# Performance work log

Measured on AMD Instinct MI355X. Metric: run time of the kernel, lower is better.

## Reference

```python
import jax, jax.numpy as jnp
import numpy as np

N_NODES = 50000
K_NEIGH = 32
D_IN = 128
D_OUT = 128
LEAKY_ALPHA = 0.2  # tf.nn.leaky_relu default


def setup_inputs() -> dict:
    key = jax.random.key(0)
    k1, k2, k3, k4 = jax.random.split(key, 4)
    glorot = lambda k, shape: jax.random.uniform(
        k, shape, jnp.float32, -1.0, 1.0) * np.sqrt(6.0 / (shape[0] + shape[1]))
    return {
        "self_vecs": jax.random.normal(k1, (N_NODES, D_IN), jnp.float32),
        "neigh_vecs": jax.random.normal(k2, (N_NODES * K_NEIGH, D_IN), jnp.float32),
        "feat_weights": glorot(k3, (D_IN, D_OUT)),
        "attn_weights": glorot(k4, (D_OUT, 1)),
        "bias": jnp.zeros((D_OUT,), jnp.float32),
        "num_neighbors": K_NEIGH,
    }


def reference(self_vecs, neigh_vecs, feat_weights, attn_weights, bias, num_neighbors):
    n = self_vecs.shape[0]
    from_neighs = neigh_vecs @ feat_weights            # [N*K, Dout]
    h_self = self_vecs @ feat_weights                  # [N, Dout]
    neigh_logits = (from_neighs @ attn_weights).reshape(n, num_neighbors)  # [N, K]
    self_logits = h_self @ attn_weights                # [N, 1]
    logits = neigh_logits + self_logits                # [N, K]
    coefs = jax.nn.softmax(jax.nn.leaky_relu(logits, LEAKY_ALPHA), axis=-1)
    # dropout rate = 0.0 -> identity
    h_neighs = jnp.einsum("nk,nkd->nd", coefs,
                          from_neighs.reshape(n, num_neighbors, -1))  # [N, Dout]
    return jax.nn.relu(h_self + h_neighs + bias)
```

## Files before the change

kernel.cpp:

```cpp
#include <hip/hip_runtime.h>


constexpr int D   = 128;
constexpr int KN  = 32;
constexpr int LDX = 136;

typedef __bf16 bf16;
typedef __attribute__((ext_vector_type(8))) __bf16 bf16x8;
typedef __attribute__((ext_vector_type(4))) float  f32x4;

__global__ void prep_kernel(const float* __restrict__ W,
                            const float* __restrict__ attn,
                            bf16* __restrict__ Wt,
                            float* __restrict__ wa)
{
  const int i = blockIdx.x * 256 + threadIdx.x;
  if (i < D * D) {
    const int n = i >> 7, k = i & 127;
    Wt[i] = (bf16)W[(k << 7) + n];
  }
  if (i < D) {
    float s = 0.f;
    for (int n = 0; n < D; ++n) s += W[i * D + n] * attn[n];
    wa[i] = s;
  }
}

__global__ __launch_bounds__(64, 3)
void gat_pass1(const float* __restrict__ selfv,
               const float* __restrict__ neighv,
               const float* __restrict__ Wfp,
               const float* __restrict__ attnv,
               const float* __restrict__ wa_g,
               float* __restrict__ ybuf,
               int nnodes, int npn, int use_ws)
{
  __shared__ __align__(16) bf16 Xs[KN * LDX];
  __shared__ __align__(16) bf16 wab[D];

  const int lane = threadIdx.x;
  const int q = lane >> 4, l15 = lane & 15;

  float wa0, wa1;
  if (use_ws) {
    float2 w2 = *(const float2*)&wa_g[2 * lane];
    wa0 = w2.x; wa1 = w2.y;
  } else {
    float s0 = 0.f, s1 = 0.f;
    for (int n = 0; n < D; ++n) {
      const float an = attnv[n];
      s0 += Wfp[(2 * lane) * D + n] * an;
      s1 += Wfp[(2 * lane + 1) * D + n] * an;
    }
    wa0 = s0; wa1 = s1;
  }
  wab[2 * lane]     = (bf16)wa0;
  wab[2 * lane + 1] = (bf16)wa1;

  const float4* neigh4 = (const float4*)neighv;
  const float2* self2  = (const float2*)selfv;
  const int base = blockIdx.x * npn;
  if (base >= nnodes) return;

  float4 st[16];
  float2 selfr;
  {
    const float4* p = neigh4 + (size_t)base * (KN * D / 4);
    #pragma unroll
    for (int c = 0; c < 8; ++c) {
      st[2 * c]     = p[2 * (lane + 64 * c)];
      st[2 * c + 1] = p[2 * (lane + 64 * c) + 1];
    }
    selfr = self2[(size_t)base * (D / 2) + lane];
  }

  for (int i = 0; i < npn; ++i) {
    const int node = base + i;
    if (node >= nnodes) break;

    #pragma unroll
    for (int c = 0; c < 8; ++c) {
      const int cc = lane + 64 * c;
      const int row = cc >> 4, c8 = cc & 15;
      const float4 va = st[2 * c], vb = st[2 * c + 1];
      bf16x8 b = { (bf16)va.x, (bf16)va.y, (bf16)va.z, (bf16)va.w,
                   (bf16)vb.x, (bf16)vb.y, (bf16)vb.z, (bf16)vb.w };
      *(bf16x8*)&Xs[row * LDX + c8 * 8] = b;
    }
    const float2 sv = selfr;

    if (i + 1 < npn && node + 1 < nnodes) {
      const float4* p = neigh4 + (size_t)(node + 1) * (KN * D / 4);
      #pragma unroll
      for (int c = 0; c < 8; ++c) {
        st[2 * c]     = p[2 * (lane + 64 * c)];
        st[2 * c + 1] = p[2 * (lane + 64 * c) + 1];
      }
      selfr = self2[(size_t)(node + 1) * (D / 2) + lane];
    }

    f32x4 acc0 = {0.f, 0.f, 0.f, 0.f}, acc1 = {0.f, 0.f, 0.f, 0.f};
    #pragma unroll
    for (int ks = 0; ks < 4; ++ks) {
      const bf16x8 B  = *(const bf16x8*)&wab[ks * 32 + q * 8];
      const bf16x8 A0 = *(const bf16x8*)&Xs[l15 * LDX + ks * 32 + q * 8];
      const bf16x8 A1 = *(const bf16x8*)&Xs[(16 + l15) * LDX + ks * 32 + q * 8];
      acc0 = __builtin_amdgcn_mfma_f32_16x16x32_bf16(A0, B, acc0, 0, 0, 0);
      acc1 = __builtin_amdgcn_mfma_f32_16x16x32_bf16(A1, B, acc1, 0, 0, 0);
    }

    float sl = sv.x * wa0 + sv.y * wa1;
    sl += __shfl_xor(sl, 1);  sl += __shfl_xor(sl, 2);  sl += __shfl_xor(sl, 4);
    sl += __shfl_xor(sl, 8);  sl += __shfl_xor(sl, 16); sl += __shfl_xor(sl, 32);

    float e0[4], e1[4], mx = -3.4e38f;
    #pragma unroll
    for (int r = 0; r < 4; ++r) {
      float t0 = acc0[r] + sl; t0 = t0 > 0.f ? t0 : 0.2f * t0;
      float t1 = acc1[r] + sl; t1 = t1 > 0.f ? t1 : 0.2f * t1;
      e0[r] = t0; e1[r] = t1;
      mx = fmaxf(mx, fmaxf(t0, t1));
    }
    mx = fmaxf(mx, __shfl_xor(mx, 16));
    mx = fmaxf(mx, __shfl_xor(mx, 32));
    float s = 0.f;
    #pragma unroll
    for (int r = 0; r < 4; ++r) {
      e0[r] = __expf(e0[r] - mx); e1[r] = __expf(e1[r] - mx);
      s += e0[r] + e1[r];
    }
    s += __shfl_xor(s, 16); s += __shfl_xor(s, 32);
    const float inv = 1.0f / s;
    #pragma unroll
    for (int r = 0; r < 4; ++r) { e0[r] *= inv; e1[r] *= inv; }

    float cf[32];
    #pragma unroll
    for (int k = 0; k < 32; ++k) {
      const int src = ((k >> 2) & 3) * 16;
      const float v = (k < 16) ? e0[k & 3] : e1[k & 3];
      cf[k] = __int_as_float(__builtin_amdgcn_readlane(__float_as_int(v), src));
    }

    float z0 = 0.f, z1 = 0.f;
    #pragma unroll
    for (int r = 0; r < 32; ++r) {
      const unsigned u = *(const unsigned*)&Xs[r * LDX + 2 * lane];
      z0 += cf[r] * __uint_as_float(u << 16);
      z1 += cf[r] * __uint_as_float(u & 0xffff0000u);
    }
    const float2 y = { sv.x + z0, sv.y + z1 };
    *(float2*)&ybuf[(size_t)node * D + 2 * lane] = y;
  }
}

__global__ __launch_bounds__(256, 2)
void gat_pass2(const bf16* __restrict__ Wt_g,
               const float* __restrict__ Wfp,
               const float* __restrict__ biasp,
               float* __restrict__ out,
               int nnodes, int use_ws)
{
  const int tid = threadIdx.x, w = tid >> 6, lane = tid & 63;
  const int q = lane >> 4, l15 = lane & 15;
  const int t = blockIdx.x * 4 + w;
  const int row0 = t * 16;
  if (row0 >= nnodes) return;

  float bv[8];
  #pragma unroll
  for (int nt = 0; nt < 8; ++nt) bv[nt] = biasp[nt * 16 + l15];

  const int arow = row0 + l15;
  const bool rv = arow < nnodes;

  f32x4 acc[8];
  #pragma unroll
  for (int nt = 0; nt < 8; ++nt) acc[nt] = (f32x4){0.f, 0.f, 0.f, 0.f};

  #pragma unroll
  for (int ks = 0; ks < 4; ++ks) {
    float a[8];
    if (rv) {
      const float4 v0 = *(const float4*)&out[(size_t)arow * D + ks * 32 + q * 8];
      const float4 v1 = *(const float4*)&out[(size_t)arow * D + ks * 32 + q * 8 + 4];
      a[0] = v0.x; a[1] = v0.y; a[2] = v0.z; a[3] = v0.w;
      a[4] = v1.x; a[5] = v1.y; a[6] = v1.z; a[7] = v1.w;
    } else {
      #pragma unroll
      for (int j = 0; j < 8; ++j) a[j] = 0.f;
    }
    bf16x8 Ah, Al;
    #pragma unroll
    for (int j = 0; j < 8; ++j) {
      const bf16 h = (bf16)a[j];
      Ah[j] = h;
      Al[j] = (bf16)(a[j] - (float)h);
    }
    #pragma unroll
    for (int nt = 0; nt < 8; ++nt) {
      bf16x8 B;
      if (use_ws) {
        B = *(const bf16x8*)&Wt_g[(nt * 16 + l15) * D + ks * 32 + q * 8];
      } else {
        #pragma unroll
        for (int j = 0; j < 8; ++j)
          B[j] = (bf16)Wfp[(size_t)(ks * 32 + q * 8 + j) * D + nt * 16 + l15];
      }
      acc[nt] = __builtin_amdgcn_mfma_f32_16x16x32_bf16(Ah, B, acc[nt], 0, 0, 0);
      acc[nt] = __builtin_amdgcn_mfma_f32_16x16x32_bf16(Al, B, acc[nt], 0, 0, 0);
    }
  }

  #pragma unroll
  for (int nt = 0; nt < 8; ++nt) {
    #pragma unroll
    for (int r = 0; r < 4; ++r) {
      const int row = row0 + q * 4 + r;
      if (row < nnodes)
        out[(size_t)row * D + nt * 16 + l15] = fmaxf(acc[nt][r] + bv[nt], 0.f);
    }
  }
}

extern "C" void kernel_launch(void* const* d_in, const int* in_sizes, int n_in,
                              void* d_out, int out_size, void* d_ws, size_t ws_size,
                              hipStream_t stream) {
  const float* selfv  = (const float*)d_in[0];
  const float* neighv = (const float*)d_in[1];
  const float* W      = (const float*)d_in[2];
  const float* attn   = (const float*)d_in[3];
  const float* biasp  = (const float*)d_in[4];
  float* out = (float*)d_out;
  const int nnodes = in_sizes[0] / D;

  const size_t need = (size_t)D * D * sizeof(bf16) + D * sizeof(float);
  const int use_ws = (ws_size >= need) ? 1 : 0;
  bf16*  Wt_g = (bf16*)d_ws;
  float* wa_g = (float*)((char*)d_ws + (size_t)D * D * sizeof(bf16));
  if (use_ws)
    prep_kernel<<<(D * D + 255) / 256, 256, 0, stream>>>(W, attn, Wt_g, wa_g);

  const int nblk = 3072;
  const int npn  = (nnodes + nblk - 1) / nblk;
  gat_pass1<<<nblk, 64, 0, stream>>>(selfv, neighv, W, attn, wa_g, out,
                                     nnodes, npn, use_ws);

  const int ntiles = (nnodes + 15) / 16;
  gat_pass2<<<(ntiles + 3) / 4, 256, 0, stream>>>(Wt_g, W, biasp, out,
                                                  nnodes, use_ws);
}
```

Measured before the change: 1.088 ms.

## Replace LDS/MFMA logit path with register-resident FP32 dot products and shuffles

```diff
diff --git a/kernel.cpp b/kernel.cpp
--- a/kernel.cpp
+++ b/kernel.cpp
@@ -1,9 +1,8 @@
 #include <hip/hip_runtime.h>
 
 
-constexpr int D   = 128;
-constexpr int KN  = 32;
-constexpr int LDX = 136;
+constexpr int D  = 128;
+constexpr int KN = 32;
 
 typedef __bf16 bf16;
 typedef __attribute__((ext_vector_type(8))) __bf16 bf16x8;
@@ -26,7 +25,7 @@
   }
 }
 
-__global__ __launch_bounds__(64, 3)
+__global__ __launch_bounds__(256, 3)
 void gat_pass1(const float* __restrict__ selfv,
                const float* __restrict__ neighv,
                const float* __restrict__ Wfp,
@@ -35,122 +34,107 @@
                float* __restrict__ ybuf,
                int nnodes, int npn, int use_ws)
 {
-  __shared__ __align__(16) bf16 Xs[KN * LDX];
-  __shared__ __align__(16) bf16 wab[D];
-
-  const int lane = threadIdx.x;
-  const int q = lane >> 4, l15 = lane & 15;
-
-  float wa0, wa1;
+  const int tid  = threadIdx.x;
+  const int w    = tid >> 6;
+  const int lane = tid & 63;
+  const int q    = lane >> 4;
+  const int l15  = lane & 15;
+
+  float wr[8];
   if (use_ws) {
-    float2 w2 = *(const float2*)&wa_g[2 * lane];
-    wa0 = w2.x; wa1 = w2.y;
+    const float4 a = *(const float4*)&wa_g[8 * l15];
+    const float4 b = *(const float4*)&wa_g[8 * l15 + 4];
+    wr[0] = a.x; wr[1] = a.y; wr[2] = a.z; wr[3] = a.w;
+    wr[4] = b.x; wr[5] = b.y; wr[6] = b.z; wr[7] = b.w;
   } else {
-    float s0 = 0.f, s1 = 0.f;
-    for (int n = 0; n < D; ++n) {
-      const float an = attnv[n];
-      s0 += Wfp[(2 * lane) * D + n] * an;
-      s1 += Wfp[(2 * lane + 1) * D + n] * an;
-    }
-    wa0 = s0; wa1 = s1;
-  }
-  wab[2 * lane]     = (bf16)wa0;
-  wab[2 * lane + 1] = (bf16)wa1;
+    #pragma unroll
+    for (int j = 0; j < 8; ++j) {
+      float s = 0.f;
+      for (int n = 0; n < D; ++n) s += Wfp[(8 * l15 + j) * D + n] * attnv[n];
+      wr[j] = s;
+    }
+  }
 
   const float4* neigh4 = (const float4*)neighv;
-  const float2* self2  = (const float2*)selfv;
-  const int base = blockIdx.x * npn;
-  if (base >= nnodes) return;
-
-  float4 st[16];
-  float2 selfr;
-  {
-    const float4* p = neigh4 + (size_t)base * (KN * D / 4);
-    #pragma unroll
-    for (int c = 0; c < 8; ++c) {
-      st[2 * c]     = p[2 * (lane + 64 * c)];
-      st[2 * c + 1] = p[2 * (lane + 64 * c) + 1];
-    }
-    selfr = self2[(size_t)base * (D / 2) + lane];
-  }
+  const float4* self4  = (const float4*)selfv;
+  const int base = (blockIdx.x * 4 + w) * npn;
 
   for (int i = 0; i < npn; ++i) {
     const int node = base + i;
     if (node >= nnodes) break;
 
-    #pragma unroll
-    for (int c = 0; c < 8; ++c) {
-      const int cc = lane + 64 * c;
-      const int row = cc >> 4, c8 = cc & 15;
-      const float4 va = st[2 * c], vb = st[2 * c + 1];
-      bf16x8 b = { (bf16)va.x, (bf16)va.y, (bf16)va.z, (bf16)va.w,
-                   (bf16)vb.x, (bf16)vb.y, (bf16)vb.z, (bf16)vb.w };
-      *(bf16x8*)&Xs[row * LDX + c8 * 8] = b;
-    }
-    const float2 sv = selfr;
-
-    if (i + 1 < npn && node + 1 < nnodes) {
-      const float4* p = neigh4 + (size_t)(node + 1) * (KN * D / 4);
+    float4 st[16];
+    const size_t nb = (size_t)node * (KN * D / 4);
+    #pragma unroll
+    for (int c = 0; c < 8; ++c) {
+      st[2 * c]     = neigh4[nb + 2 * (lane + 64 * c)];
+      st[2 * c + 1] = neigh4[nb + 2 * (lane + 64 * c) + 1];
+    }
+    const float4 s0 = self4[(size_t)node * (D / 4) + 2 * l15];
+    const float4 s1 = self4[(size_t)node * (D / 4) + 2 * l15 + 1];
+
+    float pl[8];
+    #pragma unroll
+    for (int c = 0; c < 8; ++c) {
+      const float4 a = st[2 * c], b = st[2 * c + 1];
+      pl[c] = a.x * wr[0] + a.y * wr[1] + a.z * wr[2] + a.w * wr[3]
+            + b.x * wr[4] + b.y * wr[5] + b.z * wr[6] + b.w * wr[7];
+    }
+    #pragma unroll
+    for (int m = 1; m < 16; m <<= 1)
       #pragma unroll
-      for (int c = 0; c < 8; ++c) {
-        st[2 * c]     = p[2 * (lane + 64 * c)];
-        st[2 * c + 1] = p[2 * (lane + 64 * c) + 1];
-      }
-      selfr = self2[(size_t)(node + 1) * (D / 2) + lane];
-    }
-
-    f32x4 acc0 = {0.f, 0.f, 0.f, 0.f}, acc1 = {0.f, 0.f, 0.f, 0.f};
-    #pragma unroll
-    for (int ks = 0; ks < 4; ++ks) {
-      const bf16x8 B  = *(const bf16x8*)&wab[ks * 32 + q * 8];
-      const bf16x8 A0 = *(const bf16x8*)&Xs[l15 * LDX + ks * 32 + q * 8];
-      const bf16x8 A1 = *(const bf16x8*)&Xs[(16 + l15) * LDX + ks * 32 + q * 8];
-      acc0 = __builtin_amdgcn_mfma_f32_16x16x32_bf16(A0, B, acc0, 0, 0, 0);
-      acc1 = __builtin_amdgcn_mfma_f32_16x16x32_bf16(A1, B, acc1, 0, 0, 0);
-    }
-
-    float sl = sv.x * wa0 + sv.y * wa1;
-    sl += __shfl_xor(sl, 1);  sl += __shfl_xor(sl, 2);  sl += __shfl_xor(sl, 4);
-    sl += __shfl_xor(sl, 8);  sl += __shfl_xor(sl, 16); sl += __shfl_xor(sl, 32);
-
-    float e0[4], e1[4], mx = -3.4e38f;
-    #pragma unroll
-    for (int r = 0; r < 4; ++r) {
-      float t0 = acc0[r] + sl; t0 = t0 > 0.f ? t0 : 0.2f * t0;
-      float t1 = acc1[r] + sl; t1 = t1 > 0.f ? t1 : 0.2f * t1;
-      e0[r] = t0; e1[r] = t1;
-      mx = fmaxf(mx, fmaxf(t0, t1));
+      for (int c = 0; c < 8; ++c)
+        pl[c] += __shfl_xor(pl[c], m);
+
+    float sl = s0.x * wr[0] + s0.y * wr[1] + s0.z * wr[2] + s0.w * wr[3]
+             + s1.x * wr[4] + s1.y * wr[5] + s1.z * wr[6] + s1.w * wr[7];
+    sl += __shfl_xor(sl, 1); sl += __shfl_xor(sl, 2);
+    sl += __shfl_xor(sl, 4); sl += __shfl_xor(sl, 8);
+
+    float t[8], mx = -3.4e38f;
+    #pragma unroll
+    for (int c = 0; c < 8; ++c) {
+      float v = pl[c] + sl;
+      v = v > 0.f ? v : 0.2f * v;
+      t[c] = v;
+      mx = fmaxf(mx, v);
     }
     mx = fmaxf(mx, __shfl_xor(mx, 16));
     mx = fmaxf(mx, __shfl_xor(mx, 32));
     float s = 0.f;
     #pragma unroll
-    for (int r = 0; r < 4; ++r) {
-      e0[r] = __expf(e0[r] - mx); e1[r] = __expf(e1[r] - mx);
-      s += e0[r] + e1[r];
-    }
-    s += __shfl_xor(s, 16); s += __shfl_xor(s, 32);
+    for (int c = 0; c < 8; ++c) {
+      t[c] = __expf(t[c] - mx);
+      s += t[c];
+    }
+    s += __shfl_xor(s, 16);
+    s += __shfl_xor(s, 32);
     const float inv = 1.0f / s;
-    #pragma unroll
-    for (int r = 0; r < 4; ++r) { e0[r] *= inv; e1[r] *= inv; }
-
-    float cf[32];
-    #pragma unroll
-    for (int k = 0; k < 32; ++k) {
-      const int src = ((k >> 2) & 3) * 16;
-      const float v = (k < 16) ? e0[k & 3] : e1[k & 3];
-      cf[k] = __int_as_float(__builtin_amdgcn_readlane(__float_as_int(v), src));
-    }
-
-    float z0 = 0.f, z1 = 0.f;
-    #pragma unroll
-    for (int r = 0; r < 32; ++r) {
-      const unsigned u = *(const unsigned*)&Xs[r * LDX + 2 * lane];
-      z0 += cf[r] * __uint_as_float(u << 16);
-      z1 += cf[r] * __uint_as_float(u & 0xffff0000u);
-    }
-    const float2 y = { sv.x + z0, sv.y + z1 };
-    *(float2*)&ybuf[(size_t)node * D + 2 * lane] = y;
+
+    float z[8] = {0.f, 0.f, 0.f, 0.f, 0.f, 0.f, 0.f, 0.f};
+    #pragma unroll
+    for (int c = 0; c < 8; ++c) {
+      const float4 a = st[2 * c], b = st[2 * c + 1];
+      z[0] += t[c] * a.x; z[1] += t[c] * a.y;
+      z[2] += t[c] * a.z; z[3] += t[c] * a.w;
+      z[4] += t[c] * b.x; z[5] += t[c] * b.y;
+      z[6] += t[c] * b.z; z[7] += t[c] * b.w;
+    }
+    #pragma unroll
+    for (int j = 0; j < 8; ++j) {
+      z[j] += __shfl_xor(z[j], 16);
+      z[j] += __shfl_xor(z[j], 32);
+    }
+
+    if (q == 0) {
+      const float4 y = { s0.x + inv * z[0], s0.y + inv * z[1],
+                         s0.z + inv * z[2], s0.w + inv * z[3] };
+      *(float4*)&ybuf[(size_t)node * D + 8 * l15] = y;
+    } else if (q == 1) {
+      const float4 y = { s1.x + inv * z[4], s1.y + inv * z[5],
+                         s1.z + inv * z[6], s1.w + inv * z[7] };
+      *(float4*)&ybuf[(size_t)node * D + 8 * l15 + 4] = y;
+    }
   }
 }
 
@@ -241,10 +225,10 @@
   if (use_ws)
     prep_kernel<<<(D * D + 255) / 256, 256, 0, stream>>>(W, attn, Wt_g, wa_g);
 
-  const int nblk = 3072;
-  const int npn  = (nnodes + nblk - 1) / nblk;
-  gat_pass1<<<nblk, 64, 0, stream>>>(selfv, neighv, W, attn, wa_g, out,
-                                     nnodes, npn, use_ws);
+  const int nwaves = 3072;
+  const int npn    = (nnodes + nwaves - 1) / nwaves;
+  gat_pass1<<<nwaves / 4, 256, 0, stream>>>(selfv, neighv, W, attn, wa_g, out,
+                                            nnodes, npn, use_ws);
 
   const int ntiles = (nnodes + 15) / 16;
   gat_pass2<<<(ntiles + 3) / 4, 256, 0, stream>>>(Wt_g, W, biasp, out,
```

New measurement: 1.091 ms. No clear change (+0.3%).
